# Kernel optimization log

Hardware: AMD Instinct MI355X
Metric: run time of the kernel (lower is better)

Reference implementation:

```python
import jax, jax.numpy as jnp
import numpy as np

B, L, D, G = 4, 4096, 2048, 32
GS = D // G  # group size
EPS = 1e-05


def setup_inputs() -> dict:
    key = jax.random.key(0)
    kx, = jax.random.split(key, 1)
    return {
        "x": jax.random.normal(kx, (B, L, D), dtype=jnp.float32),
        "prev_count": jnp.zeros((B,), dtype=jnp.int32),
        "prev_mean": jnp.zeros((B, G), dtype=jnp.float32),
        "prev_var": jnp.ones((B, G), dtype=jnp.float32),
        "padding_mask": jnp.ones((B, L), dtype=jnp.bool_),
        "weight": jnp.ones((D,), dtype=jnp.float32),
        "bias": jnp.zeros((D,), dtype=jnp.float32),
    }


def _timestep_norm(x, prev_count, prev_mean, prev_var, padding_mask, weight, bias):
    b, l, d = x.shape
    xg = x.reshape(b, l, G, GS).transpose(1, 0, 2, 3)  # (L, B, G, GS)
    mk = padding_mask.transpose(1, 0)                   # (L, B)
    w = weight.reshape(1, G, GS)
    bi = bias.reshape(1, G, GS)

    def step(carry, inp):
        count, mean, var = carry            # (B,), (B,G), (B,G)
        x_t, mask_t = inp                   # (B,G,GS), (B,)
        m_t = x_t.mean(axis=-1)             # per-group mean at this timestep, (B,G)
        valid = mask_t.astype(jnp.float32)[:, None]
        c_new = count + mask_t.astype(count.dtype)
        c_safe = jnp.maximum(c_new, 1).astype(jnp.float32)[:, None]
        delta = m_t - mean
        mean = mean + delta * valid / c_safe
        m2 = var * jnp.maximum(count, 1).astype(jnp.float32)[:, None]
        m2 = m2 + delta * (m_t - mean) * valid  # Welford second-moment update
        var = m2 / c_safe
        x_hat = (x_t - mean[..., None]) * jax.lax.rsqrt(var[..., None] + EPS)
        y_t = x_hat * w + bi
        return (c_new, mean, var), y_t

    (count, mean, var), ys = jax.lax.scan(step, (prev_count, prev_mean, prev_var), (xg, mk))
    y = ys.transpose(1, 0, 2, 3).reshape(b, l, d)
    return y, count, mean, var


def reference(x, prev_count, prev_mean, prev_var, padding_mask, weight, bias):
    return _timestep_norm(x, prev_count, prev_mean, prev_var, padding_mask, weight, bias)
```

## Files before the change

### kernel.cpp

```cpp
#include <hip/hip_runtime.h>

namespace {
constexpr int Bc  = 4;
constexpr int Lc  = 4096;
constexpr int Dc  = 2048;
constexpr int Gc  = 32;
constexpr int GSc = 64;
constexpr int CHUNKS = 8;
constexpr int CT = Lc / CHUNKS;
constexpr float EPSc = 1e-5f;
constexpr long long NY = (long long)Bc * Lc * Dc;
constexpr long long NM = (long long)Bc * Gc * Lc;
typedef float vfloat4 __attribute__((ext_vector_type(4)));
}

__global__ __launch_bounds__(256) void kA(const float* __restrict__ x,
                                          const int* __restrict__ mask,
                                          float* __restrict__ gmeans,
                                          double* __restrict__ part) {
    int blk = blockIdx.x, chunk = blk & (CHUNKS - 1), bg = blk >> 3;
    int b = bg >> 5, g = bg & (Gc - 1);
    int tid = threadIdx.x, rowi = tid >> 4, col4 = tid & 15;
    const long long xbase = ((long long)b * Lc + (long long)chunk * CT) * Dc + (long long)g * GSc;

    __shared__ float sm[CT];
    for (int it = 0; it < CT / 16; ++it) {
        int r = it * 16 + rowi;
        const float4 xv = *reinterpret_cast<const float4*>(x + xbase + (long long)r * Dc + col4 * 4);
        float s = xv.x + xv.y + xv.z + xv.w;
        s += __shfl_xor(s, 1);
        s += __shfl_xor(s, 2);
        s += __shfl_xor(s, 4);
        s += __shfl_xor(s, 8);
        if (col4 == 0) sm[r] = s * (1.0f / GSc);
    }
    __syncthreads();

    if (tid < CT / 4) {
        float4 mv = *reinterpret_cast<float4*>(sm + tid * 4);
        *reinterpret_cast<float4*>(gmeans + (long long)bg * Lc + chunk * CT + tid * 4) = mv;
    }

    const int* mrow = mask + (long long)b * Lc + chunk * CT;
    float v0 = sm[tid * 2], v1 = sm[tid * 2 + 1];
    int q0 = mrow[tid * 2], q1 = mrow[tid * 2 + 1];
    double ls1 = 0.0, ls2 = 0.0; int lc = 0;
    if (q0) { ls1 += v0; ls2 += (double)v0 * v0; ++lc; }
    if (q1) { ls1 += v1; ls2 += (double)v1 * v1; ++lc; }
    __shared__ double r1[256], r2[256];
    __shared__ int rc[256];
    r1[tid] = ls1; r2[tid] = ls2; rc[tid] = lc;
    __syncthreads();
    for (int off = 128; off > 0; off >>= 1) {
        if (tid < off) { r1[tid] += r1[tid + off]; r2[tid] += r2[tid + off]; rc[tid] += rc[tid + off]; }
        __syncthreads();
    }
    if (tid == 0) {
        double* p = part + ((long long)bg * CHUNKS + chunk) * 3;
        p[0] = r1[0]; p[1] = r2[0]; p[2] = (double)rc[0];
    }
}

__global__ __launch_bounds__(256) void kB(const float* __restrict__ x,
                                          const float* __restrict__ gmeans,
                                          const double* __restrict__ part,
                                          const int* __restrict__ prev_count,
                                          const float* __restrict__ prev_mean,
                                          const float* __restrict__ prev_var,
                                          const int* __restrict__ mask,
                                          const float* __restrict__ w,
                                          const float* __restrict__ bias,
                                          float* __restrict__ y,
                                          float* __restrict__ out_count,
                                          float* __restrict__ out_mean,
                                          float* __restrict__ out_var) {
    int blk = blockIdx.x, chunk = blk & (CHUNKS - 1), bg = blk >> 3;
    int b = bg >> 5, g = bg & (Gc - 1);
    int tid = threadIdx.x, rowi = tid >> 4, col4 = tid & 15;

    __shared__ float smean[CT], srstd[CT];
    __shared__ double s1[256], s2[256];
    __shared__ int sc[256];

    const float* mrow = gmeans + (long long)bg * Lc + chunk * CT;
    const int* krow = mask + (long long)b * Lc + chunk * CT;
    float v0 = mrow[tid * 2], v1 = mrow[tid * 2 + 1];
    int q0 = krow[tid * 2], q1 = krow[tid * 2 + 1];
    double ls1 = 0.0, ls2 = 0.0; int lc = 0;
    if (q0) { ls1 += v0; ls2 += (double)v0 * v0; ++lc; }
    if (q1) { ls1 += v1; ls2 += (double)v1 * v1; ++lc; }
    s1[tid] = ls1; s2[tid] = ls2; sc[tid] = lc;
    __syncthreads();
    for (int off = 1; off < 256; off <<= 1) {
        double a1 = 0.0, a2 = 0.0; int ac = 0;
        if (tid >= off) { a1 = s1[tid - off]; a2 = s2[tid - off]; ac = sc[tid - off]; }
        __syncthreads();
        s1[tid] += a1; s2[tid] += a2; sc[tid] += ac;
        __syncthreads();
    }
    double ex1 = s1[tid] - ls1, ex2 = s2[tid] - ls2;
    int exc = sc[tid] - lc;

    double c1 = 0.0, c2 = 0.0, ccnt = 0.0;
    const double* pb = part + (long long)bg * CHUNKS * 3;
    for (int c = 0; c < chunk; ++c) { c1 += pb[c * 3]; c2 += pb[c * 3 + 1]; ccnt += pb[c * 3 + 2]; }

    double c0    = (double)prev_count[b];
    double mean0 = (double)prev_mean[bg];
    double M2_0  = (double)prev_var[bg] * fmax(c0, 1.0);
    const float c0f = (float)c0, mean0f = (float)mean0, M2_0f = (float)M2_0;

    double run1 = c1 + ex1, run2 = c2 + ex2, runc = ccnt + (double)exc;
    #pragma unroll
    for (int e = 0; e < 2; ++e) {
        float vv = e ? v1 : v0;
        int qq = e ? q1 : q0;
        if (qq) { run1 += vv; run2 += (double)vv * vv; runc += 1.0; }
        float run1f = (float)run1, run2f = (float)run2, cv = (float)runc;
        float ctot = c0f + cv, csafe = fmaxf(ctot, 1.0f);
        float invcs = __builtin_amdgcn_rcpf(csafe);
        float meanT = fmaf(c0f, mean0f, run1f) * invcs;
        float M2 = M2_0f;
        if (runc > 0.0) {
            float invcv = __builtin_amdgcn_rcpf(cv);
            M2 += run2f - run1f * run1f * invcv;
            float dd = run1f * invcv - mean0f;
            M2 += dd * dd * c0f * cv * invcs;
        }
        float varT = M2 * invcs;
        smean[tid * 2 + e] = meanT;
        srstd[tid * 2 + e] = __builtin_amdgcn_rsqf(varT + EPSc);
    }

    if (chunk == CHUNKS - 1 && tid == 255) {
        double S1 = c1 + s1[255], S2 = c2 + s2[255], cv = ccnt + (double)sc[255];
        double ctot = c0 + cv, csafe = fmax(ctot, 1.0);
        double meanF = (c0 * mean0 + S1) / csafe;
        double M2 = M2_0;
        if (cv > 0.0) {
            M2 += S2 - S1 * S1 / cv;
            double dd = S1 / cv - mean0;
            M2 += dd * dd * c0 * cv / csafe;
        }
        double varF = M2 / csafe;
        if (g == 0) out_count[b] = (float)ctot;
        out_mean[bg] = (float)meanF;
        out_var[bg]  = (float)varF;
    }
    __syncthreads();

    const long long xbase = ((long long)b * Lc + (long long)chunk * CT) * Dc + (long long)g * GSc;
    float4 wv = *reinterpret_cast<const float4*>(w + g * GSc + col4 * 4);
    float4 bvv = *reinterpret_cast<const float4*>(bias + g * GSc + col4 * 4);
    for (int it = 0; it < CT / 16; ++it) {
        int r = it * 16 + rowi;
        float mean = smean[r];
        float rstd = srstd[r];
        const float4 xv = *reinterpret_cast<const float4*>(x + xbase + (long long)r * Dc + col4 * 4);
        vfloat4 yv;
        yv.x = (xv.x - mean) * rstd * wv.x + bvv.x;
        yv.y = (xv.y - mean) * rstd * wv.y + bvv.y;
        yv.z = (xv.z - mean) * rstd * wv.z + bvv.z;
        yv.w = (xv.w - mean) * rstd * wv.w + bvv.w;
        __builtin_nontemporal_store(yv, reinterpret_cast<vfloat4*>(y + xbase + (long long)r * Dc + col4 * 4));
    }
}

extern "C" void kernel_launch(void* const* d_in, const int* in_sizes, int n_in,
                              void* d_out, int out_size, void* d_ws, size_t ws_size,
                              hipStream_t stream) {
    const float* x         = (const float*)d_in[0];
    const int* prev_count  = (const int*)d_in[1];
    const float* prev_mean = (const float*)d_in[2];
    const float* prev_var  = (const float*)d_in[3];
    const int* mask        = (const int*)d_in[4];
    const float* weight    = (const float*)d_in[5];
    const float* bias      = (const float*)d_in[6];

    float* out       = (float*)d_out;
    float* y         = out;
    float* out_count = out + NY;
    float* out_mean  = out_count + Bc;
    float* out_var   = out_mean + (long long)Bc * Gc;

    float* gmeans = (float*)d_ws;
    double* part  = (double*)((char*)d_ws + NM * sizeof(float));

    const int grid = Bc * Gc * CHUNKS;
    kA<<<grid, 256, 0, stream>>>(x, mask, gmeans, part);
    kB<<<grid, 256, 0, stream>>>(x, gmeans, part, prev_count, prev_mean, prev_var,
                                 mask, weight, bias, y, out_count, out_mean, out_var);
}
```

Before: 66.23 us.

## Fuse stats and normalize into one kernel with decoupled look-back carry chain

Replaces the two-pass design (means/partials kernel, then normalize kernel that re-reads x) with a single persistent kernel. Each block holds a 512-row super-chunk of x in registers, computes the group means and the prefix scan, and receives the running sums from the previous chunk through a spin-waited sequence flag and carry in global memory. It then normalizes straight from registers. This removes the second read of x and the gmeans round trip. In exchange, the chunks of each (batch, group) chain are serialized, spin waits can stall, only 256 blocks are launched, and the 32 float4 registers per thread add heavy register pressure.

```diff
diff --git a/kernel.cpp b/kernel.cpp
--- a/kernel.cpp
+++ b/kernel.cpp
@@ -6,163 +6,162 @@
 constexpr int Dc  = 2048;
 constexpr int Gc  = 32;
 constexpr int GSc = 64;
-constexpr int CHUNKS = 8;
-constexpr int CT = Lc / CHUNKS;
+constexpr int SC  = 512;
+constexpr int NSC = Lc / SC;
 constexpr float EPSc = 1e-5f;
 constexpr long long NY = (long long)Bc * Lc * Dc;
-constexpr long long NM = (long long)Bc * Gc * Lc;
 typedef float vfloat4 __attribute__((ext_vector_type(4)));
+#define SCOPE_AGENT __HIP_MEMORY_SCOPE_AGENT
 }
 
-__global__ __launch_bounds__(256) void kA(const float* __restrict__ x,
-                                          const int* __restrict__ mask,
-                                          float* __restrict__ gmeans,
-                                          double* __restrict__ part) {
-    int blk = blockIdx.x, chunk = blk & (CHUNKS - 1), bg = blk >> 3;
-    int b = bg >> 5, g = bg & (Gc - 1);
-    int tid = threadIdx.x, rowi = tid >> 4, col4 = tid & 15;
-    const long long xbase = ((long long)b * Lc + (long long)chunk * CT) * Dc + (long long)g * GSc;
-
-    __shared__ float sm[CT];
-    for (int it = 0; it < CT / 16; ++it) {
-        int r = it * 16 + rowi;
-        const float4 xv = *reinterpret_cast<const float4*>(x + xbase + (long long)r * Dc + col4 * 4);
-        float s = xv.x + xv.y + xv.z + xv.w;
-        s += __shfl_xor(s, 1);
-        s += __shfl_xor(s, 2);
-        s += __shfl_xor(s, 4);
-        s += __shfl_xor(s, 8);
-        if (col4 == 0) sm[r] = s * (1.0f / GSc);
-    }
-    __syncthreads();
-
-    if (tid < CT / 4) {
-        float4 mv = *reinterpret_cast<float4*>(sm + tid * 4);
-        *reinterpret_cast<float4*>(gmeans + (long long)bg * Lc + chunk * CT + tid * 4) = mv;
-    }
-
-    const int* mrow = mask + (long long)b * Lc + chunk * CT;
-    float v0 = sm[tid * 2], v1 = sm[tid * 2 + 1];
-    int q0 = mrow[tid * 2], q1 = mrow[tid * 2 + 1];
-    double ls1 = 0.0, ls2 = 0.0; int lc = 0;
-    if (q0) { ls1 += v0; ls2 += (double)v0 * v0; ++lc; }
-    if (q1) { ls1 += v1; ls2 += (double)v1 * v1; ++lc; }
-    __shared__ double r1[256], r2[256];
-    __shared__ int rc[256];
-    r1[tid] = ls1; r2[tid] = ls2; rc[tid] = lc;
-    __syncthreads();
-    for (int off = 128; off > 0; off >>= 1) {
-        if (tid < off) { r1[tid] += r1[tid + off]; r2[tid] += r2[tid + off]; rc[tid] += rc[tid + off]; }
-        __syncthreads();
-    }
-    if (tid == 0) {
-        double* p = part + ((long long)bg * CHUNKS + chunk) * 3;
-        p[0] = r1[0]; p[1] = r2[0]; p[2] = (double)rc[0];
-    }
+__global__ void kInit(int* __restrict__ seq, double* __restrict__ carry) {
+    int t = threadIdx.x;
+    seq[t] = 0;
+    carry[t * 3 + 0] = 0.0;
+    carry[t * 3 + 1] = 0.0;
+    carry[t * 3 + 2] = 0.0;
 }
 
-__global__ __launch_bounds__(256) void kB(const float* __restrict__ x,
-                                          const float* __restrict__ gmeans,
-                                          const double* __restrict__ part,
-                                          const int* __restrict__ prev_count,
-                                          const float* __restrict__ prev_mean,
-                                          const float* __restrict__ prev_var,
-                                          const int* __restrict__ mask,
-                                          const float* __restrict__ w,
-                                          const float* __restrict__ bias,
-                                          float* __restrict__ y,
-                                          float* __restrict__ out_count,
-                                          float* __restrict__ out_mean,
-                                          float* __restrict__ out_var) {
-    int blk = blockIdx.x, chunk = blk & (CHUNKS - 1), bg = blk >> 3;
-    int b = bg >> 5, g = bg & (Gc - 1);
-    int tid = threadIdx.x, rowi = tid >> 4, col4 = tid & 15;
+__global__ __launch_bounds__(256, 2) void kMain(
+        const float* __restrict__ x,
+        const int* __restrict__ prev_count,
+        const float* __restrict__ prev_mean,
+        const float* __restrict__ prev_var,
+        const int* __restrict__ mask,
+        const float* __restrict__ w,
+        const float* __restrict__ bias,
+        float* __restrict__ y,
+        float* __restrict__ out_count,
+        float* __restrict__ out_mean,
+        float* __restrict__ out_var,
+        int* __restrict__ seq,
+        double* __restrict__ carry) {
+    const int blk = blockIdx.x;
+    const int bg = blk >> 1, p = blk & 1;
+    const int b = bg >> 5, g = bg & (Gc - 1);
+    const int tid = threadIdx.x;
+    const int r16 = tid >> 4, col4 = tid & 15;
 
-    __shared__ float smean[CT], srstd[CT];
+    __shared__ float  sm[SC];
+    __shared__ float  smean[SC], srstd[SC];
     __shared__ double s1[256], s2[256];
-    __shared__ int sc[256];
+    __shared__ int    scnt[256];
+    __shared__ double cLDS[3];
 
-    const float* mrow = gmeans + (long long)bg * Lc + chunk * CT;
-    const int* krow = mask + (long long)b * Lc + chunk * CT;
-    float v0 = mrow[tid * 2], v1 = mrow[tid * 2 + 1];
-    int q0 = krow[tid * 2], q1 = krow[tid * 2 + 1];
-    double ls1 = 0.0, ls2 = 0.0; int lc = 0;
-    if (q0) { ls1 += v0; ls2 += (double)v0 * v0; ++lc; }
-    if (q1) { ls1 += v1; ls2 += (double)v1 * v1; ++lc; }
-    s1[tid] = ls1; s2[tid] = ls2; sc[tid] = lc;
-    __syncthreads();
-    for (int off = 1; off < 256; off <<= 1) {
-        double a1 = 0.0, a2 = 0.0; int ac = 0;
-        if (tid >= off) { a1 = s1[tid - off]; a2 = s2[tid - off]; ac = sc[tid - off]; }
-        __syncthreads();
-        s1[tid] += a1; s2[tid] += a2; sc[tid] += ac;
-        __syncthreads();
-    }
-    double ex1 = s1[tid] - ls1, ex2 = s2[tid] - ls2;
-    int exc = sc[tid] - lc;
-
-    double c1 = 0.0, c2 = 0.0, ccnt = 0.0;
-    const double* pb = part + (long long)bg * CHUNKS * 3;
-    for (int c = 0; c < chunk; ++c) { c1 += pb[c * 3]; c2 += pb[c * 3 + 1]; ccnt += pb[c * 3 + 2]; }
-
-    double c0    = (double)prev_count[b];
-    double mean0 = (double)prev_mean[bg];
-    double M2_0  = (double)prev_var[bg] * fmax(c0, 1.0);
+    const double c0    = (double)prev_count[b];
+    const double mean0 = (double)prev_mean[bg];
+    const double M2_0  = (double)prev_var[bg] * fmax(c0, 1.0);
     const float c0f = (float)c0, mean0f = (float)mean0, M2_0f = (float)M2_0;
 
-    double run1 = c1 + ex1, run2 = c2 + ex2, runc = ccnt + (double)exc;
-    #pragma unroll
-    for (int e = 0; e < 2; ++e) {
-        float vv = e ? v1 : v0;
-        int qq = e ? q1 : q0;
-        if (qq) { run1 += vv; run2 += (double)vv * vv; runc += 1.0; }
-        float run1f = (float)run1, run2f = (float)run2, cv = (float)runc;
-        float ctot = c0f + cv, csafe = fmaxf(ctot, 1.0f);
-        float invcs = __builtin_amdgcn_rcpf(csafe);
-        float meanT = fmaf(c0f, mean0f, run1f) * invcs;
-        float M2 = M2_0f;
-        if (runc > 0.0) {
-            float invcv = __builtin_amdgcn_rcpf(cv);
-            M2 += run2f - run1f * run1f * invcv;
-            float dd = run1f * invcv - mean0f;
-            M2 += dd * dd * c0f * cv * invcs;
+    const float4 wv  = *reinterpret_cast<const float4*>(w + g * GSc + col4 * 4);
+    const float4 bvv = *reinterpret_cast<const float4*>(bias + g * GSc + col4 * 4);
+
+    for (int k = 0; k < NSC / 2; ++k) {
+        const int sc = k * 2 + p;
+        const int tbase = sc * SC;
+        const long long xbase = ((long long)b * Lc + tbase) * Dc + (long long)g * GSc + col4 * 4;
+
+        float4 xa[32];
+        #pragma unroll
+        for (int it = 0; it < 32; ++it) {
+            xa[it] = *reinterpret_cast<const float4*>(x + xbase + (long long)(it * 16 + r16) * Dc);
         }
-        float varT = M2 * invcs;
-        smean[tid * 2 + e] = meanT;
-        srstd[tid * 2 + e] = __builtin_amdgcn_rsqf(varT + EPSc);
-    }
 
-    if (chunk == CHUNKS - 1 && tid == 255) {
-        double S1 = c1 + s1[255], S2 = c2 + s2[255], cv = ccnt + (double)sc[255];
-        double ctot = c0 + cv, csafe = fmax(ctot, 1.0);
-        double meanF = (c0 * mean0 + S1) / csafe;
-        double M2 = M2_0;
-        if (cv > 0.0) {
-            M2 += S2 - S1 * S1 / cv;
-            double dd = S1 / cv - mean0;
-            M2 += dd * dd * c0 * cv / csafe;
+        #pragma unroll
+        for (int it = 0; it < 32; ++it) {
+            float s = xa[it].x + xa[it].y + xa[it].z + xa[it].w;
+            s += __shfl_xor(s, 1);
+            s += __shfl_xor(s, 2);
+            s += __shfl_xor(s, 4);
+            s += __shfl_xor(s, 8);
+            if (col4 == 0) sm[it * 16 + r16] = s * (1.0f / GSc);
         }
-        double varF = M2 / csafe;
-        if (g == 0) out_count[b] = (float)ctot;
-        out_mean[bg] = (float)meanF;
-        out_var[bg]  = (float)varF;
-    }
-    __syncthreads();
+        __syncthreads();
 
-    const long long xbase = ((long long)b * Lc + (long long)chunk * CT) * Dc + (long long)g * GSc;
-    float4 wv = *reinterpret_cast<const float4*>(w + g * GSc + col4 * 4);
-    float4 bvv = *reinterpret_cast<const float4*>(bias + g * GSc + col4 * 4);
-    for (int it = 0; it < CT / 16; ++it) {
-        int r = it * 16 + rowi;
-        float mean = smean[r];
-        float rstd = srstd[r];
-        const float4 xv = *reinterpret_cast<const float4*>(x + xbase + (long long)r * Dc + col4 * 4);
-        vfloat4 yv;
-        yv.x = (xv.x - mean) * rstd * wv.x + bvv.x;
-        yv.y = (xv.y - mean) * rstd * wv.y + bvv.y;
-        yv.z = (xv.z - mean) * rstd * wv.z + bvv.z;
-        yv.w = (xv.w - mean) * rstd * wv.w + bvv.w;
-        __builtin_nontemporal_store(yv, reinterpret_cast<vfloat4*>(y + xbase + (long long)r * Dc + col4 * 4));
+        const int* mrow = mask + (long long)b * Lc + tbase;
+        float v0 = sm[tid * 2], v1 = sm[tid * 2 + 1];
+        int q0 = mrow[tid * 2], q1 = mrow[tid * 2 + 1];
+        double ls1 = 0.0, ls2 = 0.0; int lc = 0;
+        if (q0) { ls1 += v0; ls2 += (double)v0 * v0; ++lc; }
+        if (q1) { ls1 += v1; ls2 += (double)v1 * v1; ++lc; }
+        s1[tid] = ls1; s2[tid] = ls2; scnt[tid] = lc;
+        __syncthreads();
+        for (int off = 1; off < 256; off <<= 1) {
+            double a1 = 0.0, a2 = 0.0; int ac = 0;
+            if (tid >= off) { a1 = s1[tid - off]; a2 = s2[tid - off]; ac = scnt[tid - off]; }
+            __syncthreads();
+            s1[tid] += a1; s2[tid] += a2; scnt[tid] += ac;
+            __syncthreads();
+        }
+        const double ex1 = s1[tid] - ls1, ex2 = s2[tid] - ls2;
+        const int exc = scnt[tid] - lc;
+
+        if (tid == 0) {
+            while (__hip_atomic_load(&seq[bg], __ATOMIC_ACQUIRE, SCOPE_AGENT) < sc) {
+                __builtin_amdgcn_s_sleep(2);
+            }
+            double c1   = __hip_atomic_load(&carry[bg * 3 + 0], __ATOMIC_RELAXED, SCOPE_AGENT);
+            double c2   = __hip_atomic_load(&carry[bg * 3 + 1], __ATOMIC_RELAXED, SCOPE_AGENT);
+            double ccnt = __hip_atomic_load(&carry[bg * 3 + 2], __ATOMIC_RELAXED, SCOPE_AGENT);
+            cLDS[0] = c1; cLDS[1] = c2; cLDS[2] = ccnt;
+            const double n1 = c1 + s1[255], n2 = c2 + s2[255], nc = ccnt + (double)scnt[255];
+            __hip_atomic_store(&carry[bg * 3 + 0], n1, __ATOMIC_RELAXED, SCOPE_AGENT);
+            __hip_atomic_store(&carry[bg * 3 + 1], n2, __ATOMIC_RELAXED, SCOPE_AGENT);
+            __hip_atomic_store(&carry[bg * 3 + 2], nc, __ATOMIC_RELAXED, SCOPE_AGENT);
+            __hip_atomic_store(&seq[bg], sc + 1, __ATOMIC_RELEASE, SCOPE_AGENT);
+            if (sc == NSC - 1) {
+                double ctot = c0 + nc, csafe = fmax(ctot, 1.0);
+                double meanF = (c0 * mean0 + n1) / csafe;
+                double M2 = M2_0;
+                if (nc > 0.0) {
+                    M2 += n2 - n1 * n1 / nc;
+                    double dd = n1 / nc - mean0;
+                    M2 += dd * dd * c0 * nc / csafe;
+                }
+                if (g == 0) out_count[b] = (float)ctot;
+                out_mean[bg] = (float)meanF;
+                out_var[bg]  = (float)(M2 / csafe);
+            }
+        }
+        __syncthreads();
+
+        double run1 = cLDS[0] + ex1, run2 = cLDS[1] + ex2, runc = cLDS[2] + (double)exc;
+        #pragma unroll
+        for (int e = 0; e < 2; ++e) {
+            float vv = e ? v1 : v0;
+            int qq = e ? q1 : q0;
+            if (qq) { run1 += vv; run2 += (double)vv * vv; runc += 1.0; }
+            float run1f = (float)run1, run2f = (float)run2, cv = (float)runc;
+            float ctot = c0f + cv, csafe = fmaxf(ctot, 1.0f);
+            float invcs = __builtin_amdgcn_rcpf(csafe);
+            float meanT = fmaf(c0f, mean0f, run1f) * invcs;
+            float M2 = M2_0f;
+            if (runc > 0.0) {
+                float invcv = __builtin_amdgcn_rcpf(cv);
+                M2 += run2f - run1f * run1f * invcv;
+                float dd = run1f * invcv - mean0f;
+                M2 += dd * dd * c0f * cv * invcs;
+            }
+            float varT = M2 * invcs;
+            smean[tid * 2 + e] = meanT;
+            srstd[tid * 2 + e] = __builtin_amdgcn_rsqf(varT + EPSc);
+        }
+        __syncthreads();
+
+        #pragma unroll
+        for (int it = 0; it < 32; ++it) {
+            const int r = it * 16 + r16;
+            const float mean = smean[r];
+            const float rstd = srstd[r];
+            vfloat4 yv;
+            yv.x = (xa[it].x - mean) * rstd * wv.x + bvv.x;
+            yv.y = (xa[it].y - mean) * rstd * wv.y + bvv.y;
+            yv.z = (xa[it].z - mean) * rstd * wv.z + bvv.z;
+            yv.w = (xa[it].w - mean) * rstd * wv.w + bvv.w;
+            __builtin_nontemporal_store(
+                yv, reinterpret_cast<vfloat4*>(y + xbase + (long long)(it * 16 + r16) * Dc));
+        }
+        __syncthreads();
     }
 }
 
@@ -183,11 +182,11 @@
     float* out_mean  = out_count + Bc;
     float* out_var   = out_mean + (long long)Bc * Gc;
 
-    float* gmeans = (float*)d_ws;
-    double* part  = (double*)((char*)d_ws + NM * sizeof(float));
+    double* carry = (double*)d_ws;
+    int* seq      = (int*)((char*)d_ws + 128 * 3 * sizeof(double));
 
-    const int grid = Bc * Gc * CHUNKS;
-    kA<<<grid, 256, 0, stream>>>(x, mask, gmeans, part);
-    kB<<<grid, 256, 0, stream>>>(x, gmeans, part, prev_count, prev_mean, prev_var,
-                                 mask, weight, bias, y, out_count, out_mean, out_var);
+    kInit<<<1, 128, 0, stream>>>(seq, carry);
+    kMain<<<Bc * Gc * 2, 256, 0, stream>>>(x, prev_count, prev_mean, prev_var,
+                                           mask, weight, bias, y,
+                                           out_count, out_mean, out_var, seq, carry);
 }
```

Measured after the change: 103.2 us. 55.8% more time.

## Fuse stats and normalize passes into one cooperative kernel with grid sync

Applied to the files above, without the earlier changes.

Replaces the two-kernel pipeline (group-mean pass, then scan and normalize pass) with a single cooperative kernel of 512 blocks. Each block handles two time chunks in sequence: it computes chunk means, does a block-level prefix scan, publishes the chunk partials, grid-syncs, and then normalizes while the x tile is likely still in cache. This removes the second kernel launch and the gmeans round trip through global memory. The cost is two grid-wide barriers and a host-side occupancy query on every call, with the old two-kernel path kept as a fallback.

```diff
diff --git a/kernel.cpp b/kernel.cpp
--- a/kernel.cpp
+++ b/kernel.cpp
@@ -1,4 +1,7 @@
 #include <hip/hip_runtime.h>
+#include <hip/hip_cooperative_groups.h>
+
+namespace cg = cooperative_groups;
 
 namespace {
 constexpr int Bc  = 4;
@@ -6,12 +9,162 @@
 constexpr int Dc  = 2048;
 constexpr int Gc  = 32;
 constexpr int GSc = 64;
-constexpr int CHUNKS = 8;
-constexpr int CT = Lc / CHUNKS;
 constexpr float EPSc = 1e-5f;
 constexpr long long NY = (long long)Bc * Lc * Dc;
 constexpr long long NM = (long long)Bc * Gc * Lc;
+constexpr int CTc = 512;
+constexpr int NCc = Lc / CTc;
+constexpr int JBc = NCc / 2;
+constexpr int CHUNKS = 8;
+constexpr int CT2 = Lc / CHUNKS;
 typedef float vfloat4 __attribute__((ext_vector_type(4)));
+}
+
+__global__ __launch_bounds__(256, 4) void kCoop(
+        const float* __restrict__ x,
+        const int* __restrict__ prev_count,
+        const float* __restrict__ prev_mean,
+        const float* __restrict__ prev_var,
+        const int* __restrict__ mask,
+        const float* __restrict__ w,
+        const float* __restrict__ bias,
+        float* __restrict__ y,
+        float* __restrict__ out_count,
+        float* __restrict__ out_mean,
+        float* __restrict__ out_var,
+        double* __restrict__ part) {
+    cg::grid_group grid = cg::this_grid();
+
+    const int blk = blockIdx.x;
+    const int bg = blk >> 2, j = blk & 3;
+    const int b = bg >> 5, g = bg & (Gc - 1);
+    const int tid = threadIdx.x;
+    const int r16 = tid >> 4, col4 = tid & 15;
+
+    __shared__ float  sm[CTc];
+    __shared__ float  smean[CTc], srstd[CTc];
+    __shared__ double s1[256], s2[256];
+    __shared__ int    scnt[256];
+    __shared__ double cLDS[3];
+
+    const double c0    = (double)prev_count[b];
+    const double mean0 = (double)prev_mean[bg];
+    const double M2_0  = (double)prev_var[bg] * fmax(c0, 1.0);
+    const float c0f = (float)c0, mean0f = (float)mean0, M2_0f = (float)M2_0;
+
+    const float4 wv  = *reinterpret_cast<const float4*>(w + g * GSc + col4 * 4);
+    const float4 bvv = *reinterpret_cast<const float4*>(bias + g * GSc + col4 * 4);
+
+    for (int phase = 0; phase < 2; ++phase) {
+        const int c = j + phase * JBc;
+        const int tbase = c * CTc;
+        const long long xbase = ((long long)b * Lc + tbase) * Dc + (long long)g * GSc + col4 * 4;
+
+        for (int it = 0; it < CTc / 16; ++it) {
+            const int r = it * 16 + r16;
+            const float4 xv = *reinterpret_cast<const float4*>(x + xbase + (long long)r * Dc);
+            float s = xv.x + xv.y + xv.z + xv.w;
+            s += __shfl_xor(s, 1);
+            s += __shfl_xor(s, 2);
+            s += __shfl_xor(s, 4);
+            s += __shfl_xor(s, 8);
+            if (col4 == 0) sm[r] = s * (1.0f / GSc);
+        }
+        __syncthreads();
+
+        const int* mrow = mask + (long long)b * Lc + tbase;
+        const float v0 = sm[2 * tid], v1 = sm[2 * tid + 1];
+        const int q0 = mrow[2 * tid], q1 = mrow[2 * tid + 1];
+        double ls1 = 0.0, ls2 = 0.0; int lc = 0;
+        if (q0) { ls1 += v0; ls2 += (double)v0 * v0; ++lc; }
+        if (q1) { ls1 += v1; ls2 += (double)v1 * v1; ++lc; }
+        s1[tid] = ls1; s2[tid] = ls2; scnt[tid] = lc;
+        __syncthreads();
+        for (int off = 1; off < 256; off <<= 1) {
+            double a1 = 0.0, a2 = 0.0; int ac = 0;
+            if (tid >= off) { a1 = s1[tid - off]; a2 = s2[tid - off]; ac = scnt[tid - off]; }
+            __syncthreads();
+            s1[tid] += a1; s2[tid] += a2; scnt[tid] += ac;
+            __syncthreads();
+        }
+        const double ex1 = s1[tid] - ls1, ex2 = s2[tid] - ls2;
+        const int exc = scnt[tid] - lc;
+
+        if (tid == 255) {
+            double* p = part + (long long)(bg * NCc + c) * 3;
+            p[0] = s1[255]; p[1] = s2[255]; p[2] = (double)scnt[255];
+        }
+
+        grid.sync();
+
+        if (tid < 64) {
+            double a1 = 0.0, a2 = 0.0, ac = 0.0;
+            if (tid < c) {
+                const double* p = part + (long long)(bg * NCc + tid) * 3;
+                a1 = p[0]; a2 = p[1]; ac = p[2];
+            }
+            #pragma unroll
+            for (int o = 1; o < 8; o <<= 1) {
+                a1 += __shfl_xor(a1, o);
+                a2 += __shfl_xor(a2, o);
+                ac += __shfl_xor(ac, o);
+            }
+            if (tid == 0) { cLDS[0] = a1; cLDS[1] = a2; cLDS[2] = ac; }
+        }
+        __syncthreads();
+
+        double run1 = cLDS[0] + ex1, run2 = cLDS[1] + ex2, runc = cLDS[2] + (double)exc;
+        #pragma unroll
+        for (int e = 0; e < 2; ++e) {
+            const float vv = e ? v1 : v0;
+            const int qq = e ? q1 : q0;
+            if (qq) { run1 += vv; run2 += (double)vv * vv; runc += 1.0; }
+            float run1f = (float)run1, run2f = (float)run2, cv = (float)runc;
+            float ctot = c0f + cv, csafe = fmaxf(ctot, 1.0f);
+            float invcs = __builtin_amdgcn_rcpf(csafe);
+            float meanT = fmaf(c0f, mean0f, run1f) * invcs;
+            float M2 = M2_0f;
+            if (runc > 0.0) {
+                float invcv = __builtin_amdgcn_rcpf(cv);
+                M2 += run2f - run1f * run1f * invcv;
+                float dd = run1f * invcv - mean0f;
+                M2 += dd * dd * c0f * cv * invcs;
+            }
+            float varT = M2 * invcs;
+            smean[2 * tid + e] = meanT;
+            srstd[2 * tid + e] = __builtin_amdgcn_rsqf(varT + EPSc);
+        }
+
+        if (c == NCc - 1 && tid == 255) {
+            double ctot = c0 + runc, csafe = fmax(ctot, 1.0);
+            double meanF = (c0 * mean0 + run1) / csafe;
+            double M2 = M2_0;
+            if (runc > 0.0) {
+                M2 += run2 - run1 * run1 / runc;
+                double dd = run1 / runc - mean0;
+                M2 += dd * dd * c0 * runc / csafe;
+            }
+            if (g == 0) out_count[b] = (float)ctot;
+            out_mean[bg] = (float)meanF;
+            out_var[bg]  = (float)(M2 / csafe);
+        }
+        __syncthreads();
+
+        for (int it = 0; it < CTc / 16; ++it) {
+            const int r = it * 16 + r16;
+            const float mean = smean[r];
+            const float rstd = srstd[r];
+            const float4 xv = *reinterpret_cast<const float4*>(x + xbase + (long long)r * Dc);
+            vfloat4 yv;
+            yv.x = (xv.x - mean) * rstd * wv.x + bvv.x;
+            yv.y = (xv.y - mean) * rstd * wv.y + bvv.y;
+            yv.z = (xv.z - mean) * rstd * wv.z + bvv.z;
+            yv.w = (xv.w - mean) * rstd * wv.w + bvv.w;
+            __builtin_nontemporal_store(
+                yv, reinterpret_cast<vfloat4*>(y + xbase + (long long)r * Dc));
+        }
+        __syncthreads();
+    }
 }
 
 __global__ __launch_bounds__(256) void kA(const float* __restrict__ x,
@@ -21,10 +174,10 @@
     int blk = blockIdx.x, chunk = blk & (CHUNKS - 1), bg = blk >> 3;
     int b = bg >> 5, g = bg & (Gc - 1);
     int tid = threadIdx.x, rowi = tid >> 4, col4 = tid & 15;
-    const long long xbase = ((long long)b * Lc + (long long)chunk * CT) * Dc + (long long)g * GSc;
-
-    __shared__ float sm[CT];
-    for (int it = 0; it < CT / 16; ++it) {
+    const long long xbase = ((long long)b * Lc + (long long)chunk * CT2) * Dc + (long long)g * GSc;
+
+    __shared__ float sm[CT2];
+    for (int it = 0; it < CT2 / 16; ++it) {
         int r = it * 16 + rowi;
         const float4 xv = *reinterpret_cast<const float4*>(x + xbase + (long long)r * Dc + col4 * 4);
         float s = xv.x + xv.y + xv.z + xv.w;
@@ -36,12 +189,12 @@
     }
     __syncthreads();
 
-    if (tid < CT / 4) {
+    if (tid < CT2 / 4) {
         float4 mv = *reinterpret_cast<float4*>(sm + tid * 4);
-        *reinterpret_cast<float4*>(gmeans + (long long)bg * Lc + chunk * CT + tid * 4) = mv;
-    }
-
-    const int* mrow = mask + (long long)b * Lc + chunk * CT;
+        *reinterpret_cast<float4*>(gmeans + (long long)bg * Lc + chunk * CT2 + tid * 4) = mv;
+    }
+
+    const int* mrow = mask + (long long)b * Lc + chunk * CT2;
     float v0 = sm[tid * 2], v1 = sm[tid * 2 + 1];
     int q0 = mrow[tid * 2], q1 = mrow[tid * 2 + 1];
     double ls1 = 0.0, ls2 = 0.0; int lc = 0;
@@ -78,12 +231,12 @@
     int b = bg >> 5, g = bg & (Gc - 1);
     int tid = threadIdx.x, rowi = tid >> 4, col4 = tid & 15;
 
-    __shared__ float smean[CT], srstd[CT];
+    __shared__ float smean[CT2], srstd[CT2];
     __shared__ double s1[256], s2[256];
     __shared__ int sc[256];
 
-    const float* mrow = gmeans + (long long)bg * Lc + chunk * CT;
-    const int* krow = mask + (long long)b * Lc + chunk * CT;
+    const float* mrow = gmeans + (long long)bg * Lc + chunk * CT2;
+    const int* krow = mask + (long long)b * Lc + chunk * CT2;
     float v0 = mrow[tid * 2], v1 = mrow[tid * 2 + 1];
     int q0 = krow[tid * 2], q1 = krow[tid * 2 + 1];
     double ls1 = 0.0, ls2 = 0.0; int lc = 0;
@@ -149,10 +302,10 @@
     }
     __syncthreads();
 
-    const long long xbase = ((long long)b * Lc + (long long)chunk * CT) * Dc + (long long)g * GSc;
+    const long long xbase = ((long long)b * Lc + (long long)chunk * CT2) * Dc + (long long)g * GSc;
     float4 wv = *reinterpret_cast<const float4*>(w + g * GSc + col4 * 4);
     float4 bvv = *reinterpret_cast<const float4*>(bias + g * GSc + col4 * 4);
-    for (int it = 0; it < CT / 16; ++it) {
+    for (int it = 0; it < CT2 / 16; ++it) {
         int r = it * 16 + rowi;
         float mean = smean[r];
         float rstd = srstd[r];
@@ -162,7 +315,8 @@
         yv.y = (xv.y - mean) * rstd * wv.y + bvv.y;
         yv.z = (xv.z - mean) * rstd * wv.z + bvv.z;
         yv.w = (xv.w - mean) * rstd * wv.w + bvv.w;
-        __builtin_nontemporal_store(yv, reinterpret_cast<vfloat4*>(y + xbase + (long long)r * Dc + col4 * 4));
+        __builtin_nontemporal_store(
+            yv, reinterpret_cast<vfloat4*>(y + xbase + (long long)r * Dc + col4 * 4));
     }
 }
 
@@ -183,11 +337,27 @@
     float* out_mean  = out_count + Bc;
     float* out_var   = out_mean + (long long)Bc * Gc;
 
-    float* gmeans = (float*)d_ws;
-    double* part  = (double*)((char*)d_ws + NM * sizeof(float));
-
-    const int grid = Bc * Gc * CHUNKS;
-    kA<<<grid, 256, 0, stream>>>(x, mask, gmeans, part);
-    kB<<<grid, 256, 0, stream>>>(x, gmeans, part, prev_count, prev_mean, prev_var,
-                                 mask, weight, bias, y, out_count, out_mean, out_var);
-}
+    double* partC = (double*)d_ws;
+    float* gmeans = (float*)((char*)d_ws + 32768);
+    double* partF = (double*)((char*)d_ws + 32768 + NM * sizeof(float));
+
+    int blocksPerCU = 0;
+    (void)hipOccupancyMaxActiveBlocksPerMultiprocessor(&blocksPerCU, kCoop, 256, 0);
+    const int coopGrid = Bc * Gc * JBc;
+    bool useCoop = ((long long)blocksPerCU * 256 >= coopGrid);
+
+    if (useCoop) {
+        void* args[] = {
+            (void*)&x, (void*)&prev_count, (void*)&prev_mean, (void*)&prev_var,
+            (void*)&mask, (void*)&weight, (void*)&bias, (void*)&y,
+            (void*)&out_count, (void*)&out_mean, (void*)&out_var, (void*)&partC
+        };
+        hipError_t e = hipLaunchCooperativeKernel((void*)kCoop, dim3(coopGrid), dim3(256),
+                                                  args, 0, stream);
+        if (e == hipSuccess) return;
+    }
+    kA<<<Bc * Gc * CHUNKS, 256, 0, stream>>>(x, mask, gmeans, partF);
+    kB<<<Bc * Gc * CHUNKS, 256, 0, stream>>>(x, gmeans, partF, prev_count, prev_mean,
+                                             prev_var, mask, weight, bias, y,
+                                             out_count, out_mean, out_var);
+}
```

New measurement: 224.7 us. +239.2%, slower.
